# Kernel tuning notes

Measured on AMD Instinct MI355X. Metric: run time of the kernel, lower is better.

## Reference

```python
import jax, jax.numpy as jnp
import numpy as np

B, T, H, W, E, V, K = 16, 64, 16, 32, 256, 128, 3
NUM_BLOCKS = 3


def setup_inputs() -> dict:
    key = jax.random.key(0)
    ks = jax.random.split(key, 8)
    sc = 0.05  # keep logits moderate
    return {
        "encoder_output": jax.random.normal(ks[0], (B, H, W, E), jnp.float32),
        "decoder_input": jax.random.normal(ks[1], (B, H, W, E), jnp.float32),
        "labels": jax.random.randint(ks[2], (B, T), 0, V),
        "embed_table": (jax.random.normal(ks[3], (V, E), jnp.float32) * sc),
        "conv_w": (jax.random.normal(ks[4], (K, E, 2 * E), jnp.float32) * sc),  # ConvTBC weight [k, Cin, Cout]
        "conv_b": jnp.zeros((2 * E,), jnp.float32),
        "W_w": (jax.random.normal(ks[5], (E, E), jnp.float32) * sc),   # Linear(out/2 -> E), torch layout [out,in]
        "W_b": jnp.zeros((E,), jnp.float32),
        "Wo_w": (jax.random.normal(ks[6], (V, E), jnp.float32) * sc),  # Linear(E -> V)
        "Wo_b": jnp.zeros((V,), jnp.float32),
    }


def reference(encoder_output, decoder_input, embed_table, conv_w, conv_b,
              W_w, W_b, Wo_w, Wo_b, labels):
    # Work in [B, T, C]; the torch code's TBC transposes are layout-only.
    s = embed_table[labels]                     # [B, T, E]  (s in original, kept fixed)
    a = s                                       # a_l
    dec_flat = decoder_input.reshape(B, H * W, E)            # [B, HW, E]
    residual = (encoder_output + decoder_input).reshape(B, H * W, E)  # [B, HW, E]

    for _ in range(NUM_BLOCKS):
        # ConvTBC: 1D conv over T, weight [k, Cin, Cout]
        conv = jax.lax.conv_general_dilated(
            a, conv_w, window_strides=(1,), padding=((K // 2, K // 2),),
            dimension_numbers=("NWC", "WIO", "NWC")) + conv_b   # [B, T, 2E]
        # GLU over channel dim
        za, zb = jnp.split(conv, 2, axis=-1)
        z = za * jax.nn.sigmoid(zb)                              # [B, T, E]
        h = z @ W_w.T + W_b + s                                  # [B, T, E]
        # exp / sum over spatial positions == softmax over HW (same math, stable)
        scores = jnp.einsum("bte,bse->bts", h, dec_flat)         # [B, T, HW]
        alpha = jax.nn.softmax(scores, axis=2)
        # weighted sum of residual (avoids the [B,T,HW,E] repeat)
        c = jnp.einsum("bts,bse->bte", alpha, residual)          # [B, T, E]
        a = c + z

    logits = a @ Wo_w.T + Wo_b                                   # [B, T, V]
    return jax.nn.log_softmax(logits, axis=2)


if __name__ == "__main__":
    out = reference(**setup_inputs())
    print(out.shape)
```

## Files before the change

kernel.cpp:

```cpp
#include <hip/hip_runtime.h>
#include <hip/hip_bf16.h>
#include <math.h>

#define BB 16
#define TT 64
#define HWXY 512
#define EE 256
#define VV 128

typedef __bf16 bf16x8 __attribute__((ext_vector_type(8)));
typedef unsigned short u16x8 __attribute__((ext_vector_type(8)));
typedef float f32x4 __attribute__((ext_vector_type(4)));

__device__ __forceinline__ f32x4 mfma16(bf16x8 a, bf16x8 b, f32x4 c) {
    return __builtin_amdgcn_mfma_f32_16x16x32_bf16(a, b, c, 0, 0, 0);
}

__device__ __forceinline__ unsigned short f2bf(float f) {
    union { float f; unsigned int i; } v; v.f = f;
    unsigned int x = v.i;
    return (unsigned short)((x + 0x7fffu + ((x >> 16) & 1u)) >> 16);
}

__device__ __forceinline__ float bf2f(unsigned short u) {
    union { unsigned int i; float f; } v; v.i = ((unsigned int)u) << 16;
    return v.f;
}

__device__ __forceinline__ u16x8 pack8(float4 v0, float4 v1) {
    u16x8 o;
    o[0] = f2bf(v0.x); o[1] = f2bf(v0.y); o[2] = f2bf(v0.z); o[3] = f2bf(v0.w);
    o[4] = f2bf(v1.x); o[5] = f2bf(v1.y); o[6] = f2bf(v1.z); o[7] = f2bf(v1.w);
    return o;
}

__device__ __forceinline__ void dma16(const void* g, void* l) {
    __builtin_amdgcn_global_load_lds(
        (const __attribute__((address_space(1))) void*)g,
        (__attribute__((address_space(3))) void*)l, 16, 0, 0);
}

#define VMWAIT0() do { asm volatile("s_waitcnt vmcnt(0)" ::: "memory"); \
                       __builtin_amdgcn_sched_barrier(0); } while (0)

__global__ __launch_bounds__(256) void k_setup(
    const float* __restrict__ enc, const float* __restrict__ dec,
    const int* __restrict__ labels, const float* __restrict__ embed,
    const float* __restrict__ conv_w, const float* __restrict__ W_w,
    const float* __restrict__ Wo_w,
    unsigned short* __restrict__ s_bf, unsigned short* __restrict__ a_bf,
    unsigned short* __restrict__ dec_bf, unsigned short* __restrict__ resT,
    unsigned short* __restrict__ convwT, unsigned short* __restrict__ WT,
    unsigned short* __restrict__ Wo_bf) {
    __shared__ unsigned short tl[64][66];
    int bid = blockIdx.x;
    if (bid < 512) {
        const int b = bid >> 5, rem = bid & 31;
        const int s0 = (rem >> 2) << 6, e0 = (rem & 3) << 6;
#pragma unroll
        for (int it = 0; it < 16; ++it) {
            int lin = threadIdx.x + it * 256;
            int sl = lin >> 6, el = lin & 63;
            int src = (b * HWXY + s0 + sl) * EE + e0 + el;
            float dv = dec[src];
            dec_bf[src] = f2bf(dv);
            tl[sl][el] = f2bf(enc[src] + dv);
        }
        __syncthreads();
#pragma unroll
        for (int it = 0; it < 16; ++it) {
            int lin = threadIdx.x + it * 256;
            int el = lin >> 6, sl = lin & 63;
            resT[(b * EE + e0 + el) * HWXY + s0 + sl] = tl[sl][el];
        }
        return;
    }
    bid -= 512;
    if (bid < 96) {
        const int c0 = (bid >> 3) << 6, j0 = (bid & 7) << 6;
#pragma unroll
        for (int it = 0; it < 16; ++it) {
            int lin = threadIdx.x + it * 256;
            int cl = lin >> 6, jl = lin & 63;
            tl[cl][jl] = f2bf(conv_w[(c0 + cl) * 512 + j0 + jl]);
        }
        __syncthreads();
#pragma unroll
        for (int it = 0; it < 16; ++it) {
            int lin = threadIdx.x + it * 256;
            int jl = lin >> 6, cl = lin & 63;
            convwT[(j0 + jl) * 768 + c0 + cl] = tl[cl][jl];
        }
        return;
    }
    bid -= 96;
    if (bid < 16) {
        const int c0 = (bid >> 2) << 6, j0 = (bid & 3) << 6;
#pragma unroll
        for (int it = 0; it < 16; ++it) {
            int lin = threadIdx.x + it * 256;
            int cl = lin >> 6, jl = lin & 63;
            tl[cl][jl] = f2bf(W_w[(c0 + cl) * 256 + j0 + jl]);
        }
        __syncthreads();
#pragma unroll
        for (int it = 0; it < 16; ++it) {
            int lin = threadIdx.x + it * 256;
            int el = lin >> 6, pl = lin & 63;
            WT[(j0 + el) * 256 + c0 + pl] = tl[pl][el];
        }
        return;
    }
    bid -= 16;
    int i8 = (bid * 256 + threadIdx.x) * 8;
    const int n1 = BB * TT * EE;
    if (i8 < n1) {
        int b = i8 >> 14, t = (i8 >> 8) & 63, e = i8 & 255;
        int lab = labels[b * TT + t];
        const float* ep = embed + lab * EE + e;
        float4 v0 = *(const float4*)ep, v1 = *(const float4*)(ep + 4);
        u16x8 p = pack8(v0, v1);
        *(u16x8*)(s_bf + i8) = p;
        *(u16x8*)(a_bf + i8) = p;
        return;
    }
    i8 -= n1;
    float4 v0 = *(const float4*)(Wo_w + i8), v1 = *(const float4*)(Wo_w + i8 + 4);
    *(u16x8*)(Wo_bf + i8) = pack8(v0, v1);
}

__global__ __launch_bounds__(256) void k_precomp(
    const unsigned short* __restrict__ dec_bf, const unsigned short* __restrict__ WT,
    const unsigned short* __restrict__ s_bf, const float* __restrict__ W_b,
    unsigned short* __restrict__ G, float* __restrict__ base_g) {
    __shared__ __align__(16) char smem[98304];
    char* const As = smem;
    char* const Bs = smem + 32768;
    const int tid = threadIdx.x;
    const int w = tid >> 6, L = tid & 63, l16 = L & 15, lg = L >> 4;
    int bid = blockIdx.x;

    if (bid < 256) {
        const int b = bid >> 4, st = (bid >> 1) & 7, et = bid & 1;
#pragma unroll
        for (int i = 0; i < 8; ++i) {
            const int p = w * 8 + i;
            const int r = 2 * p + (L >> 5);
            dma16(dec_bf + (b * HWXY + st * 64 + r) * EE + (((L & 31) ^ (r & 7)) << 3),
                  As + p * 1024);
        }
#pragma unroll
        for (int i = 0; i < 16; ++i) {
            const int slot = w * 16 + i;
            const int kc = slot >> 3, nf = slot & 7;
            dma16(WT + (et * 128 + nf * 16 + l16) * EE + kc * 32 + lg * 8,
                  Bs + slot * 1024);
        }
        VMWAIT0();
        __syncthreads();
        f32x4 acc[4][2] = {{{0,0,0,0},{0,0,0,0}},{{0,0,0,0},{0,0,0,0}},
                           {{0,0,0,0},{0,0,0,0}},{{0,0,0,0},{0,0,0,0}}};
#pragma unroll
        for (int kc = 0; kc < 8; ++kc) {
#pragma unroll
            for (int m = 0; m < 4; ++m) {
                const int arow = m * 16 + l16;
                const bf16x8 af = *(const bf16x8*)(
                    As + arow * 512 + (((kc * 4 + lg) ^ (arow & 7)) << 4));
                acc[m][0] = mfma16(af, *(const bf16x8*)(Bs + (kc * 8 + w * 2) * 1024 + L * 16), acc[m][0]);
                acc[m][1] = mfma16(af, *(const bf16x8*)(Bs + (kc * 8 + w * 2 + 1) * 1024 + L * 16), acc[m][1]);
            }
        }
#pragma unroll
        for (int m = 0; m < 4; ++m)
#pragma unroll
            for (int nf = 0; nf < 2; ++nf)
#pragma unroll
                for (int j = 0; j < 4; ++j) {
                    const int s = st * 64 + m * 16 + lg * 4 + j;
                    const int e = et * 128 + w * 32 + nf * 16 + l16;
                    G[(b * HWXY + s) * EE + e] = f2bf(acc[m][nf][j]);
                }
    } else {
        bid -= 256;
        const int b = bid >> 3, st = bid & 7;
#pragma unroll
        for (int it = 0; it < 8; ++it) {
            int unit = tid + it * 256;
            int row = unit >> 5, ch = unit & 31;
            u16x8 v = *(const u16x8*)(s_bf + (b * TT + row) * EE + ch * 8);
            u16x8 o;
#pragma unroll
            for (int k = 0; k < 8; ++k) o[k] = f2bf(bf2f(v[k]) + W_b[ch * 8 + k]);
            *(u16x8*)(As + row * 512 + ((ch ^ (row & 7)) << 4)) = o;
        }
#pragma unroll
        for (int i = 0; i < 8; ++i) {
            const int slot = w * 8 + i;
            const int kc = slot >> 2, nf = slot & 3;
            dma16(dec_bf + (b * HWXY + st * 64 + nf * 16 + l16) * EE + kc * 32 + lg * 8,
                  Bs + slot * 1024);
        }
        VMWAIT0();
        __syncthreads();
        f32x4 acc[4] = {{0,0,0,0},{0,0,0,0},{0,0,0,0},{0,0,0,0}};
        const int arow = w * 16 + l16;
#pragma unroll
        for (int kc = 0; kc < 8; ++kc) {
            const bf16x8 af = *(const bf16x8*)(
                As + arow * 512 + (((kc * 4 + lg) ^ (arow & 7)) << 4));
#pragma unroll
            for (int nf = 0; nf < 4; ++nf)
                acc[nf] = mfma16(af, *(const bf16x8*)(Bs + (kc * 4 + nf) * 1024 + L * 16), acc[nf]);
        }
#pragma unroll
        for (int nf = 0; nf < 4; ++nf)
#pragma unroll
            for (int j = 0; j < 4; ++j) {
                const int t = w * 16 + lg * 4 + j;
                base_g[(b * TT + t) * HWXY + st * 64 + nf * 16 + l16] = acc[nf][j];
            }
    }
}

__global__ __launch_bounds__(256) void k_conv(
    const unsigned short* __restrict__ a_in, const unsigned short* __restrict__ convwT,
    const float* __restrict__ conv_b, unsigned short* __restrict__ z_bf) {
    __shared__ __align__(16) char As[33792];
    __shared__ __align__(16) char Bs[49152];
    const int ct = blockIdx.x, b = blockIdx.y;
    const int tid = threadIdx.x;
    const int w = tid >> 6, L = tid & 63, l16 = L & 15, lg = L >> 4;

#pragma unroll
    for (int i = 0; i < 12; ++i) {
        const int slot = w * 12 + i;
        const int kc = slot >> 1, half = slot & 1;
        dma16(convwT + (ct * 16 + l16 + half * 256) * 768 + kc * 32 + lg * 8,
              Bs + slot * 1024);
    }
#pragma unroll
    for (int i = 0; i < 8; ++i) {
        const int p = w * 8 + i;
        const int r = 1 + 2 * p + (L >> 5);
        dma16(a_in + (b * TT + r - 1) * EE + (((L & 31) ^ (r & 7)) << 3),
              As + 512 + p * 1024);
    }
    if (tid < 64) {
        char* dst = (tid < 32) ? (As + tid * 16) : (As + 65 * 512 + (tid - 32) * 16);
        *(u16x8*)dst = (u16x8){0,0,0,0,0,0,0,0};
    }
    VMWAIT0();
    __syncthreads();

    f32x4 za = {0,0,0,0}, zb = {0,0,0,0};
#pragma unroll
    for (int kt = 0; kt < 3; ++kt) {
        const int arow = w * 16 + l16 + kt;
        const char* ab = As + arow * 512;
        const int swz = (arow & 7) << 4;
#pragma unroll
        for (int ec = 0; ec < 8; ++ec) {
            const bf16x8 af = *(const bf16x8*)(ab + ((ec * 64 + lg * 16) ^ swz));
            const int kc = kt * 8 + ec;
            za = mfma16(af, *(const bf16x8*)(Bs + (kc * 2) * 1024 + L * 16), za);
            zb = mfma16(af, *(const bf16x8*)(Bs + (kc * 2 + 1) * 1024 + L * 16), zb);
        }
    }
    const int p = ct * 16 + l16;
    const float cbA = conv_b[p], cbB = conv_b[p + 256];
#pragma unroll
    for (int j = 0; j < 4; ++j) {
        const int t = w * 16 + lg * 4 + j;
        const float v = za[j] + cbA, u = zb[j] + cbB;
        z_bf[(b * TT + t) * EE + p] = f2bf(v / (1.0f + __expf(-u)));
    }
}

__global__ __launch_bounds__(256) void k_scores(
    const unsigned short* __restrict__ z_bf, const unsigned short* __restrict__ G,
    const float* __restrict__ base_g, unsigned short* __restrict__ p_bf,
    float* __restrict__ m_part, float* __restrict__ s_part) {
    __shared__ __align__(16) char Zs[32768];
    __shared__ __align__(16) char Gs[16384];
    __shared__ float basel[64 * 36];
    const int st = blockIdx.x, b = blockIdx.y;
    const int tid = threadIdx.x;
    const int w = tid >> 6, L = tid & 63, l16 = L & 15, lg = L >> 4;

#pragma unroll
    for (int i = 0; i < 8; ++i) {
        const int p = w * 8 + i;
        const int r = 2 * p + (L >> 5);
        dma16(z_bf + (b * TT + r) * EE + (((L & 31) ^ (r & 7)) << 3), Zs + p * 1024);
    }
#pragma unroll
    for (int i = 0; i < 4; ++i) {
        const int slot = w * 4 + i;
        const int kc = slot >> 1, nf = slot & 1;
        dma16(G + (b * HWXY + st * 32 + nf * 16 + l16) * EE + kc * 32 + lg * 8,
              Gs + slot * 1024);
    }
    {
        const int row = tid >> 2, c0 = (tid & 3) * 8;
        const float* src = base_g + (b * TT + row) * HWXY + st * 32 + c0;
        float4 v0 = *(const float4*)src, v1 = *(const float4*)(src + 4);
        *(float4*)(basel + row * 36 + c0) = v0;
        *(float4*)(basel + row * 36 + c0 + 4) = v1;
    }
    VMWAIT0();
    __syncthreads();

    f32x4 sc[2] = {{0,0,0,0},{0,0,0,0}};
    const int arow = w * 16 + l16;
#pragma unroll
    for (int kc = 0; kc < 8; ++kc) {
        const bf16x8 af = *(const bf16x8*)(
            Zs + arow * 512 + (((kc * 4 + lg) ^ (arow & 7)) << 4));
        sc[0] = mfma16(af, *(const bf16x8*)(Gs + (kc * 2) * 1024 + L * 16), sc[0]);
        sc[1] = mfma16(af, *(const bf16x8*)(Gs + (kc * 2 + 1) * 1024 + L * 16), sc[1]);
    }
    float pm[4], ps[4];
#pragma unroll
    for (int j = 0; j < 4; ++j) {
        const int row = w * 16 + lg * 4 + j;
        sc[0][j] += basel[row * 36 + l16];
        sc[1][j] += basel[row * 36 + 16 + l16];
        float m = fmaxf(sc[0][j], sc[1][j]);
#pragma unroll
        for (int off = 8; off >= 1; off >>= 1) m = fmaxf(m, __shfl_xor(m, off));
        pm[j] = m;
        const float p0 = __expf(sc[0][j] - m);
        const float p1 = __expf(sc[1][j] - m);
        sc[0][j] = p0; sc[1][j] = p1;
        float s = p0 + p1;
#pragma unroll
        for (int off = 8; off >= 1; off >>= 1) s += __shfl_xor(s, off);
        ps[j] = s;
    }
    if (l16 == 0) {
#pragma unroll
        for (int j = 0; j < 4; ++j) {
            const int t = w * 16 + lg * 4 + j;
            m_part[(b * 16 + st) * TT + t] = pm[j];
            s_part[(b * 16 + st) * TT + t] = ps[j];
        }
    }
#pragma unroll
    for (int nf = 0; nf < 2; ++nf)
#pragma unroll
        for (int j = 0; j < 4; ++j) {
            const int t = w * 16 + lg * 4 + j;
            p_bf[(b * TT + t) * HWXY + st * 32 + nf * 16 + l16] = f2bf(sc[nf][j]);
        }
}

__global__ __launch_bounds__(256) void k_attn(
    const unsigned short* __restrict__ p_bf, const unsigned short* __restrict__ resT,
    const unsigned short* __restrict__ z_bf, const float* __restrict__ m_part,
    const float* __restrict__ s_part, unsigned short* __restrict__ a_out) {
    __shared__ __align__(16) char Ps[32768];
    __shared__ __align__(16) char Bs[32768];
    __shared__ unsigned short Zr[1024];
    __shared__ float mp[512], sp[512];
    const int et = blockIdx.x, tt = blockIdx.y, b = blockIdx.z;
    const int tid = threadIdx.x;
    const int w = tid >> 6, L = tid & 63, l16 = L & 15, lg = L >> 4;

#pragma unroll
    for (int i = 0; i < 8; ++i) {
        const int r = w * 8 + i;
        dma16(p_bf + (b * TT + tt * 32 + r) * HWXY + ((L ^ (r & 7)) << 3), Ps + r * 1024);
    }
#pragma unroll
    for (int i = 0; i < 8; ++i) {
        const int slot = w * 8 + i;
        const int kc = slot >> 1, nf = slot & 1;
        dma16(resT + (b * EE + et * 32 + nf * 16 + l16) * HWXY + kc * 32 + lg * 8,
              Bs + slot * 1024);
    }
    {
        if (tid < 128) {
            const int t = tid >> 2, part = tid & 3;
            *(u16x8*)(Zr + t * 32 + part * 8) =
                *(const u16x8*)(z_bf + (b * TT + tt * 32 + t) * EE + et * 32 + part * 8);
        }
        const int stl = tid >> 5, tl = tid & 31;
        mp[tid] = m_part[(b * 16 + stl) * TT + tt * 32 + tl];
        sp[tid] = s_part[(b * 16 + stl) * TT + tt * 32 + tl];
        mp[tid + 256] = m_part[(b * 16 + stl + 8) * TT + tt * 32 + tl];
        sp[tid + 256] = s_part[(b * 16 + stl + 8) * TT + tt * 32 + tl];
    }
    VMWAIT0();
    __syncthreads();

    const int mg = w >> 1, nh = w & 1;
    float corr[4][16];
#pragma unroll
    for (int j = 0; j < 4; ++j) {
        const int row = mg * 16 + lg * 4 + j;
        float mgl = mp[row];
#pragma unroll
        for (int s = 1; s < 16; ++s) mgl = fmaxf(mgl, mp[s * 32 + row]);
        float S = 0.f;
#pragma unroll
        for (int s = 0; s < 16; ++s) {
            const float c = __expf(mp[s * 32 + row] - mgl);
            corr[j][s] = c;
            S += sp[s * 32 + row] * c;
        }
        const float is = 1.0f / S;
#pragma unroll
        for (int s = 0; s < 16; ++s) corr[j][s] *= is;
    }

    f32x4 ca = {0,0,0,0};
    const int arow = mg * 16 + l16;
#pragma unroll
    for (int st = 0; st < 16; ++st) {
        const bf16x8 af = *(const bf16x8*)(
            Ps + arow * 1024 + (((st * 4 + lg) ^ (arow & 7)) << 4));
        f32x4 t0 = mfma16(af, *(const bf16x8*)(Bs + (st * 2 + nh) * 1024 + L * 16),
                          (f32x4){0,0,0,0});
#pragma unroll
        for (int j = 0; j < 4; ++j) ca[j] += t0[j] * corr[j][st];
    }
#pragma unroll
    for (int j = 0; j < 4; ++j) {
        const int row = mg * 16 + lg * 4 + j;
        const int t = tt * 32 + row;
        a_out[(b * TT + t) * EE + et * 32 + nh * 16 + l16] =
            f2bf(ca[j] + bf2f(Zr[row * 32 + nh * 16 + l16]));
    }
}

__global__ __launch_bounds__(256) void k_logits(
    const unsigned short* __restrict__ a_bf, const unsigned short* __restrict__ Wo_bf,
    const float* __restrict__ Wo_b, float* __restrict__ out) {
    __shared__ __align__(16) char As[8192];
    __shared__ __align__(16) char Ws[65536];
    __shared__ float red_m[64], red_s[64];
    const int tt = blockIdx.x, b = blockIdx.y;
    const int tid = threadIdx.x;
    const int w = tid >> 6, L = tid & 63, l16 = L & 15, lg = L >> 4;

#pragma unroll
    for (int i = 0; i < 2; ++i) {
        const int p = w * 2 + i;
        const int row = p * 2 + (L >> 5);
        dma16(a_bf + (b * TT + tt * 16 + row) * EE + (((L & 31) ^ (row & 7)) << 3),
              As + p * 1024);
    }
#pragma unroll
    for (int i = 0; i < 16; ++i) {
        const int slot = w * 16 + i;
        const int kc = slot >> 3, vg = slot & 7;
        dma16(Wo_bf + (vg * 16 + l16) * EE + kc * 32 + lg * 8, Ws + slot * 1024);
    }
    VMWAIT0();
    __syncthreads();

    f32x4 l0 = {0,0,0,0}, l1 = {0,0,0,0};
#pragma unroll
    for (int kc = 0; kc < 8; ++kc) {
        const bf16x8 af = *(const bf16x8*)(As + l16 * 512 + ((kc * 64 + lg * 16) ^ ((l16 & 7) << 4)));
        l0 = mfma16(af, *(const bf16x8*)(Ws + (kc * 8 + w * 2) * 1024 + L * 16), l0);
        l1 = mfma16(af, *(const bf16x8*)(Ws + (kc * 8 + w * 2 + 1) * 1024 + L * 16), l1);
    }
    const int v0 = w * 32 + l16, v1 = v0 + 16;
    const float wb0 = Wo_b[v0], wb1 = Wo_b[v1];
    float lv0[4], lv1[4], mg[4];
#pragma unroll
    for (int j = 0; j < 4; ++j) {
        lv0[j] = l0[j] + wb0;
        lv1[j] = l1[j] + wb1;
        float m = fmaxf(lv0[j], lv1[j]);
#pragma unroll
        for (int off = 8; off >= 1; off >>= 1) m = fmaxf(m, __shfl_xor(m, off));
        if (l16 == 0) red_m[(lg * 4 + j) * 4 + w] = m;
    }
    __syncthreads();
#pragma unroll
    for (int j = 0; j < 4; ++j) {
        const int row = lg * 4 + j;
        float m = red_m[row * 4 + 0];
#pragma unroll
        for (int ww = 1; ww < 4; ++ww) m = fmaxf(m, red_m[row * 4 + ww]);
        mg[j] = m;
        float s = __expf(lv0[j] - m) + __expf(lv1[j] - m);
#pragma unroll
        for (int off = 8; off >= 1; off >>= 1) s += __shfl_xor(s, off);
        if (l16 == 0) red_s[row * 4 + w] = s;
    }
    __syncthreads();
#pragma unroll
    for (int j = 0; j < 4; ++j) {
        const int row = lg * 4 + j;
        float s = red_s[row * 4 + 0] + red_s[row * 4 + 1] + red_s[row * 4 + 2] + red_s[row * 4 + 3];
        const float lse = mg[j] + __logf(s);
        const int gt = b * TT + tt * 16 + row;
        out[gt * VV + v0] = lv0[j] - lse;
        out[gt * VV + v1] = lv1[j] - lse;
    }
}

extern "C" void kernel_launch(void* const* d_in, const int* in_sizes, int n_in,
                              void* d_out, int out_size, void* d_ws, size_t ws_size,
                              hipStream_t stream) {
    const float* enc    = (const float*)d_in[0];
    const float* dec    = (const float*)d_in[1];
    const int*   labels = (const int*)d_in[2];
    const float* embed  = (const float*)d_in[3];
    const float* conv_w = (const float*)d_in[4];
    const float* conv_b = (const float*)d_in[5];
    const float* W_w    = (const float*)d_in[6];
    const float* W_b    = (const float*)d_in[7];
    const float* Wo_w   = (const float*)d_in[8];
    const float* Wo_b   = (const float*)d_in[9];
    float* out = (float*)d_out;
    char* ws = (char*)d_ws;

    unsigned short* a0     = (unsigned short*)(ws + 0x000000);
    unsigned short* a1     = (unsigned short*)(ws + 0x080000);
    unsigned short* s_bf   = (unsigned short*)(ws + 0x100000);
    unsigned short* dec_bf = (unsigned short*)(ws + 0x180000);
    unsigned short* resT   = (unsigned short*)(ws + 0x580000);
    unsigned short* convwT = (unsigned short*)(ws + 0x980000);
    unsigned short* WT     = (unsigned short*)(ws + 0xA40000);
    unsigned short* Wo_bf  = (unsigned short*)(ws + 0xA60000);
    unsigned short* z_bf   = (unsigned short*)(ws + 0xA80000);
    unsigned short* p_bf   = (unsigned short*)(ws + 0xB00000);
    float*          m_part = (float*)(ws + 0xC00000);
    float*          s_part = (float*)(ws + 0xC10000);
    float*          base_g = (float*)(ws + 0xC20000);
    unsigned short* G      = (unsigned short*)(ws + 0xE20000);

    k_setup<<<768, 256, 0, stream>>>(enc, dec, labels, embed, conv_w, W_w, Wo_w,
                                     s_bf, a0, dec_bf, resT, convwT, WT, Wo_bf);
    k_precomp<<<384, 256, 0, stream>>>(dec_bf, WT, s_bf, W_b, G, base_g);

    unsigned short* ain = a0;
    unsigned short* aout = a1;
    for (int l = 0; l < 3; ++l) {
        k_conv<<<dim3(16, 16), 256, 0, stream>>>(ain, convwT, conv_b, z_bf);
        k_scores<<<dim3(16, 16), 256, 0, stream>>>(z_bf, G, base_g, p_bf, m_part, s_part);
        k_attn<<<dim3(8, 2, 16), 256, 0, stream>>>(p_bf, resT, z_bf, m_part, s_part, aout);
        unsigned short* tmp = ain; ain = aout; aout = tmp;
    }
    k_logits<<<dim3(4, 16), 256, 0, stream>>>(ain, Wo_bf, Wo_b, out);
}
```

Baseline: 77.77 us.

## Fold first-layer conv into precompute kernel and reorder grid to batch-major

Adds extra blocks to k_precomp that compute the first block's ConvTBC+GLU directly from s_bf. This removes one k_conv launch, and the a0 copy in setup is no longer written. All kernels also swap grid dimensions so the batch index is blockIdx.x, which changes how blocks are scheduled and may affect cache locality. The fused blocks run in parallel with the precompute GEMMs, which removes one serial kernel step, at the cost of a larger precompute grid.

```diff
diff --git a/kernel.cpp b/kernel.cpp
--- a/kernel.cpp
+++ b/kernel.cpp
@@ -11,6 +11,7 @@
 typedef __bf16 bf16x8 __attribute__((ext_vector_type(8)));
 typedef unsigned short u16x8 __attribute__((ext_vector_type(8)));
 typedef float f32x4 __attribute__((ext_vector_type(4)));
+typedef unsigned short u16;
 
 __device__ __forceinline__ f32x4 mfma16(bf16x8 a, bf16x8 b, f32x4 c) {
     return __builtin_amdgcn_mfma_f32_16x16x32_bf16(a, b, c, 0, 0, 0);
@@ -48,10 +49,8 @@
     const int* __restrict__ labels, const float* __restrict__ embed,
     const float* __restrict__ conv_w, const float* __restrict__ W_w,
     const float* __restrict__ Wo_w,
-    unsigned short* __restrict__ s_bf, unsigned short* __restrict__ a_bf,
-    unsigned short* __restrict__ dec_bf, unsigned short* __restrict__ resT,
-    unsigned short* __restrict__ convwT, unsigned short* __restrict__ WT,
-    unsigned short* __restrict__ Wo_bf) {
+    u16* __restrict__ s_bf, u16* __restrict__ dec_bf, u16* __restrict__ resT,
+    u16* __restrict__ convwT, u16* __restrict__ WT, u16* __restrict__ Wo_bf) {
     __shared__ unsigned short tl[64][66];
     int bid = blockIdx.x;
     if (bid < 512) {
@@ -119,9 +118,7 @@
         int lab = labels[b * TT + t];
         const float* ep = embed + lab * EE + e;
         float4 v0 = *(const float4*)ep, v1 = *(const float4*)(ep + 4);
-        u16x8 p = pack8(v0, v1);
-        *(u16x8*)(s_bf + i8) = p;
-        *(u16x8*)(a_bf + i8) = p;
+        *(u16x8*)(s_bf + i8) = pack8(v0, v1);
         return;
     }
     i8 -= n1;
@@ -130,9 +127,11 @@
 }
 
 __global__ __launch_bounds__(256) void k_precomp(
-    const unsigned short* __restrict__ dec_bf, const unsigned short* __restrict__ WT,
-    const unsigned short* __restrict__ s_bf, const float* __restrict__ W_b,
-    unsigned short* __restrict__ G, float* __restrict__ base_g) {
+    const u16* __restrict__ dec_bf, const u16* __restrict__ WT,
+    const u16* __restrict__ s_bf, const float* __restrict__ W_b,
+    u16* __restrict__ G, float* __restrict__ base_g,
+    const u16* __restrict__ convwT, const float* __restrict__ conv_b,
+    u16* __restrict__ z_bf) {
     __shared__ __align__(16) char smem[98304];
     char* const As = smem;
     char* const Bs = smem + 32768;
@@ -181,7 +180,9 @@
                     const int e = et * 128 + w * 32 + nf * 16 + l16;
                     G[(b * HWXY + s) * EE + e] = f2bf(acc[m][nf][j]);
                 }
-    } else {
+        return;
+    }
+    if (bid < 384) {
         bid -= 256;
         const int b = bid >> 3, st = bid & 7;
 #pragma unroll
@@ -220,15 +221,65 @@
                 const int t = w * 16 + lg * 4 + j;
                 base_g[(b * TT + t) * HWXY + st * 64 + nf * 16 + l16] = acc[nf][j];
             }
+        return;
+    }
+    {
+        bid -= 384;
+        const int ct = bid >> 4, b = bid & 15;
+        char* const Ac = smem;
+        char* const Bc = smem + 33792;
+#pragma unroll
+        for (int i = 0; i < 12; ++i) {
+            const int slot = w * 12 + i;
+            const int kc = slot >> 1, half = slot & 1;
+            dma16(convwT + (ct * 16 + l16 + half * 256) * 768 + kc * 32 + lg * 8,
+                  Bc + slot * 1024);
+        }
+#pragma unroll
+        for (int i = 0; i < 8; ++i) {
+            const int p = w * 8 + i;
+            const int r = 1 + 2 * p + (L >> 5);
+            dma16(s_bf + (b * TT + r - 1) * EE + (((L & 31) ^ (r & 7)) << 3),
+                  Ac + 512 + p * 1024);
+        }
+        if (tid < 64) {
+            char* dst = (tid < 32) ? (Ac + tid * 16) : (Ac + 65 * 512 + (tid - 32) * 16);
+            *(u16x8*)dst = (u16x8){0,0,0,0,0,0,0,0};
+        }
+        VMWAIT0();
+        __syncthreads();
+
+        f32x4 za = {0,0,0,0}, zb = {0,0,0,0};
+#pragma unroll
+        for (int kt = 0; kt < 3; ++kt) {
+            const int arow = w * 16 + l16 + kt;
+            const char* ab = Ac + arow * 512;
+            const int swz = (arow & 7) << 4;
+#pragma unroll
+            for (int ec = 0; ec < 8; ++ec) {
+                const bf16x8 af = *(const bf16x8*)(ab + ((ec * 64 + lg * 16) ^ swz));
+                const int kc = kt * 8 + ec;
+                za = mfma16(af, *(const bf16x8*)(Bc + (kc * 2) * 1024 + L * 16), za);
+                zb = mfma16(af, *(const bf16x8*)(Bc + (kc * 2 + 1) * 1024 + L * 16), zb);
+            }
+        }
+        const int p = ct * 16 + l16;
+        const float cbA = conv_b[p], cbB = conv_b[p + 256];
+#pragma unroll
+        for (int j = 0; j < 4; ++j) {
+            const int t = w * 16 + lg * 4 + j;
+            const float v = za[j] + cbA, u = zb[j] + cbB;
+            z_bf[(b * TT + t) * EE + p] = f2bf(v / (1.0f + __expf(-u)));
+        }
     }
 }
 
 __global__ __launch_bounds__(256) void k_conv(
-    const unsigned short* __restrict__ a_in, const unsigned short* __restrict__ convwT,
-    const float* __restrict__ conv_b, unsigned short* __restrict__ z_bf) {
+    const u16* __restrict__ a_in, const u16* __restrict__ convwT,
+    const float* __restrict__ conv_b, u16* __restrict__ z_bf) {
     __shared__ __align__(16) char As[33792];
     __shared__ __align__(16) char Bs[49152];
-    const int ct = blockIdx.x, b = blockIdx.y;
+    const int b = blockIdx.x, ct = blockIdx.y;
     const int tid = threadIdx.x;
     const int w = tid >> 6, L = tid & 63, l16 = L & 15, lg = L >> 4;
 
@@ -278,13 +329,13 @@
 }
 
 __global__ __launch_bounds__(256) void k_scores(
-    const unsigned short* __restrict__ z_bf, const unsigned short* __restrict__ G,
-    const float* __restrict__ base_g, unsigned short* __restrict__ p_bf,
+    const u16* __restrict__ z_bf, const u16* __restrict__ G,
+    const float* __restrict__ base_g, u16* __restrict__ p_bf,
     float* __restrict__ m_part, float* __restrict__ s_part) {
     __shared__ __align__(16) char Zs[32768];
     __shared__ __align__(16) char Gs[16384];
     __shared__ float basel[64 * 36];
-    const int st = blockIdx.x, b = blockIdx.y;
+    const int b = blockIdx.x, st = blockIdx.y;
     const int tid = threadIdx.x;
     const int w = tid >> 6, L = tid & 63, l16 = L & 15, lg = L >> 4;
 
@@ -356,14 +407,14 @@
 }
 
 __global__ __launch_bounds__(256) void k_attn(
-    const unsigned short* __restrict__ p_bf, const unsigned short* __restrict__ resT,
-    const unsigned short* __restrict__ z_bf, const float* __restrict__ m_part,
-    const float* __restrict__ s_part, unsigned short* __restrict__ a_out) {
+    const u16* __restrict__ p_bf, const u16* __restrict__ resT,
+    const u16* __restrict__ z_bf, const float* __restrict__ m_part,
+    const float* __restrict__ s_part, u16* __restrict__ a_out) {
     __shared__ __align__(16) char Ps[32768];
     __shared__ __align__(16) char Bs[32768];
-    __shared__ unsigned short Zr[1024];
+    __shared__ u16 Zr[1024];
     __shared__ float mp[512], sp[512];
-    const int et = blockIdx.x, tt = blockIdx.y, b = blockIdx.z;
+    const int b = blockIdx.x, et = blockIdx.y, tt = blockIdx.z;
     const int tid = threadIdx.x;
     const int w = tid >> 6, L = tid & 63, l16 = L & 15, lg = L >> 4;
 
@@ -435,12 +486,12 @@
 }
 
 __global__ __launch_bounds__(256) void k_logits(
-    const unsigned short* __restrict__ a_bf, const unsigned short* __restrict__ Wo_bf,
+    const u16* __restrict__ a_bf, const u16* __restrict__ Wo_bf,
     const float* __restrict__ Wo_b, float* __restrict__ out) {
     __shared__ __align__(16) char As[8192];
     __shared__ __align__(16) char Ws[65536];
     __shared__ float red_m[64], red_s[64];
-    const int tt = blockIdx.x, b = blockIdx.y;
+    const int b = blockIdx.x, tt = blockIdx.y;
     const int tid = threadIdx.x;
     const int w = tid >> 6, L = tid & 63, l16 = L & 15, lg = L >> 4;
 
@@ -520,32 +571,36 @@
     float* out = (float*)d_out;
     char* ws = (char*)d_ws;
 
-    unsigned short* a0     = (unsigned short*)(ws + 0x000000);
-    unsigned short* a1     = (unsigned short*)(ws + 0x080000);
-    unsigned short* s_bf   = (unsigned short*)(ws + 0x100000);
-    unsigned short* dec_bf = (unsigned short*)(ws + 0x180000);
-    unsigned short* resT   = (unsigned short*)(ws + 0x580000);
-    unsigned short* convwT = (unsigned short*)(ws + 0x980000);
-    unsigned short* WT     = (unsigned short*)(ws + 0xA40000);
-    unsigned short* Wo_bf  = (unsigned short*)(ws + 0xA60000);
-    unsigned short* z_bf   = (unsigned short*)(ws + 0xA80000);
-    unsigned short* p_bf   = (unsigned short*)(ws + 0xB00000);
-    float*          m_part = (float*)(ws + 0xC00000);
-    float*          s_part = (float*)(ws + 0xC10000);
-    float*          base_g = (float*)(ws + 0xC20000);
-    unsigned short* G      = (unsigned short*)(ws + 0xE20000);
+    u16*   a0     = (u16*)(ws + 0x000000);
+    u16*   a1     = (u16*)(ws + 0x080000);
+    u16*   s_bf   = (u16*)(ws + 0x100000);
+    u16*   dec_bf = (u16*)(ws + 0x180000);
+    u16*   resT   = (u16*)(ws + 0x580000);
+    u16*   convwT = (u16*)(ws + 0x980000);
+    u16*   WT     = (u16*)(ws + 0xA40000);
+    u16*   Wo_bf  = (u16*)(ws + 0xA60000);
+    u16*   z_bf   = (u16*)(ws + 0xA80000);
+    u16*   p_bf   = (u16*)(ws + 0xB00000);
+    float* m_part = (float*)(ws + 0xC00000);
+    float* s_part = (float*)(ws + 0xC10000);
+    float* base_g = (float*)(ws + 0xC20000);
+    u16*   G      = (u16*)(ws + 0xE20000);
 
     k_setup<<<768, 256, 0, stream>>>(enc, dec, labels, embed, conv_w, W_w, Wo_w,
-                                     s_bf, a0, dec_bf, resT, convwT, WT, Wo_bf);
-    k_precomp<<<384, 256, 0, stream>>>(dec_bf, WT, s_bf, W_b, G, base_g);
-
-    unsigned short* ain = a0;
-    unsigned short* aout = a1;
-    for (int l = 0; l < 3; ++l) {
-        k_conv<<<dim3(16, 16), 256, 0, stream>>>(ain, convwT, conv_b, z_bf);
-        k_scores<<<dim3(16, 16), 256, 0, stream>>>(z_bf, G, base_g, p_bf, m_part, s_part);
-        k_attn<<<dim3(8, 2, 16), 256, 0, stream>>>(p_bf, resT, z_bf, m_part, s_part, aout);
-        unsigned short* tmp = ain; ain = aout; aout = tmp;
-    }
-    k_logits<<<dim3(4, 16), 256, 0, stream>>>(ain, Wo_bf, Wo_b, out);
-}
+                                     s_bf, dec_bf, resT, convwT, WT, Wo_bf);
+    k_precomp<<<640, 256, 0, stream>>>(dec_bf, WT, s_bf, W_b, G, base_g,
+                                       convwT, conv_b, z_bf);
+
+    k_scores<<<dim3(16, 16), 256, 0, stream>>>(z_bf, G, base_g, p_bf, m_part, s_part);
+    k_attn<<<dim3(16, 8, 2), 256, 0, stream>>>(p_bf, resT, z_bf, m_part, s_part, a1);
+
+    k_conv<<<dim3(16, 16), 256, 0, stream>>>(a1, convwT, conv_b, z_bf);
+    k_scores<<<dim3(16, 16), 256, 0, stream>>>(z_bf, G, base_g, p_bf, m_part, s_part);
+    k_attn<<<dim3(16, 8, 2), 256, 0, stream>>>(p_bf, resT, z_bf, m_part, s_part, a0);
+
+    k_conv<<<dim3(16, 16), 256, 0, stream>>>(a0, convwT, conv_b, z_bf);
+    k_scores<<<dim3(16, 16), 256, 0, stream>>>(z_bf, G, base_g, p_bf, m_part, s_part);
+    k_attn<<<dim3(16, 8, 2), 256, 0, stream>>>(p_bf, resT, z_bf, m_part, s_part, a1);
+
+    k_logits<<<dim3(16, 4), 256, 0, stream>>>(a1, Wo_bf, Wo_b, out);
+}
```

Measured after the change: 66.31 us, median of 2. -14.7%, faster.
